# Optimization experiments

Measured on AMD Instinct MI355X. Metric: run time of the kernel, lower is better.

## Reference

```python
import jax, jax.numpy as jnp
import numpy as np


def _lstm(x_seq, W, U, b, h0, c0):
    """Keras-default LSTM. x_seq: [B,T,F]. Gate order i,f,g,o.
    Returns (all hidden states [B,T,H], final h [B,H], final c [B,H])."""
    H = U.shape[0]
    # precompute input projections for all timesteps: [T,B,4H]
    xz = jnp.einsum('btf,fg->tbg', x_seq, W) + b

    def step(carry, xz_t):
        h, c = carry
        z = xz_t + h @ U  # [B,4H]
        i = jax.nn.sigmoid(z[:, 0 * H:1 * H])
        f = jax.nn.sigmoid(z[:, 1 * H:2 * H])
        g = jnp.tanh(z[:, 2 * H:3 * H])
        o = jax.nn.sigmoid(z[:, 3 * H:4 * H])
        c = f * c + i * g
        h = o * jnp.tanh(c)
        return (h, c), h

    (hT, cT), hs = jax.lax.scan(step, (h0, c0), xz)
    return jnp.transpose(hs, (1, 0, 2)), hT, cT  # [B,T,H], [B,H], [B,H]


def setup_inputs() -> dict:
    key = jax.random.key(0)
    ks = jax.random.split(key, 7)
    B, T, F, H, C = 128, 512, 128, 512, 10
    s_in1 = 1.0 / np.sqrt(F)
    s_h = 1.0 / np.sqrt(H)
    return {
        'x': jax.random.normal(ks[0], (B, T, F), jnp.float32),
        'W1': jax.random.normal(ks[1], (F, 4 * H), jnp.float32) * s_in1,
        'U1': jax.random.normal(ks[2], (H, 4 * H), jnp.float32) * s_h,
        'b1': jnp.zeros((4 * H,), jnp.float32),
        'W2': jax.random.normal(ks[3], (H, 4 * H), jnp.float32) * s_h,
        'U2': jax.random.normal(ks[4], (H, 4 * H), jnp.float32) * s_h,
        'b2': jnp.zeros((4 * H,), jnp.float32),
        'Wd': jax.random.normal(ks[5], (H, C), jnp.float32) * s_h,
        'bd': jnp.zeros((C,), jnp.float32),
    }


def reference(x, W1, U1, b1, W2, U2, b2, Wd, bd):
    B = x.shape[0]
    H = U1.shape[0]
    h0 = jnp.zeros((B, H), x.dtype)
    c0 = jnp.zeros((B, H), x.dtype)
    # lstm1: return_sequences + return_state
    seq, h1, c1 = _lstm(x, W1, U1, b1, h0, c0)
    # Keras RNN called on [seq, h, c] uses (h, c) as lstm2's initial state
    _, h2, _ = _lstm(seq, W2, U2, b2, h1, c1)
    logits = h2 @ Wd + bd
    return jax.nn.softmax(logits, axis=-1)
```

## Files before the change

### kernel.cpp

```cpp
#include <hip/hip_runtime.h>
#include <math.h>

#define BB 128
#define TT 512
#define FF 128
#define HH 512
#define NR 2048
#define HB (HH*BB)
#define FLS 16

typedef __attribute__((ext_vector_type(8))) short short8;
typedef __attribute__((ext_vector_type(4))) float f32x4;
typedef unsigned int uint;
typedef unsigned short ushort;
typedef unsigned long long u64;

#define MFMA __builtin_amdgcn_mfma_f32_16x16x32_bf16
#define AT_LD(p)   __hip_atomic_load((p), __ATOMIC_RELAXED, __HIP_MEMORY_SCOPE_AGENT)
#define AT_ST(p,v) __hip_atomic_store((p), (v), __ATOMIC_RELAXED, __HIP_MEMORY_SCOPE_AGENT)
#define PLD(p)     (*(p))

__device__ __forceinline__ ushort f2bf(float f) {
  uint u = __float_as_uint(f);
  u += 0x7fff + ((u >> 16) & 1);
  return (ushort)(u >> 16);
}
__device__ __forceinline__ float bfh(ushort h) { return __uint_as_float(((uint)h) << 16); }
__device__ __forceinline__ u64 pk2f(float a, float b) {
  return ((u64)__float_as_uint(b) << 32) | (u64)__float_as_uint(a);
}
__device__ __forceinline__ float ftanh(float v) {
  float t = __expf(2.f * v);
  return 1.f - 2.f / (t + 1.f);
}
__device__ __forceinline__ void split8(const uint* w, short8& bh, short8& bl) {
  union { short8 v; uint d[4]; } H, Lo;
#pragma unroll
  for (int d = 0; d < 4; ++d) {
    H.d[d]  = __builtin_amdgcn_perm(w[2 * d + 1], w[2 * d], 0x07060302u);
    Lo.d[d] = __builtin_amdgcn_perm(w[2 * d + 1], w[2 * d], 0x05040100u);
  }
  bh = H.v; bl = Lo.v;
}


__global__ __launch_bounds__(256) void k_zero(float* __restrict__ p, int n) {
  int i = blockIdx.x * 256 + threadIdx.x;
  if (i < n) p[i] = 0.f;
}

__global__ __launch_bounds__(256) void k_rearr_b(const float* __restrict__ src,
                                                 float* __restrict__ dst) {
  int idx = blockIdx.x * 256 + threadIdx.x;
  int j = idx & 511, g = idx >> 9;
  dst[j * 4 + g] = src[idx];
}

__global__ __launch_bounds__(256) void k_pack_A(const float* __restrict__ src,
                                                ushort* __restrict__ dst, int ktsh) {
  int idx = blockIdx.x * 256 + threadIdx.x;
  int KTm1 = (1 << ktsh) - 1;
  int j8 = idx & 7;
  int L = (idx >> 3) & 63;
  int kt = (idx >> 9) & KTm1;
  int jb = idx >> (9 + ktsh);
  int k = kt * 32 + (L >> 4) * 8 + j8;
  int m = L & 15;
  int j = jb * 4 + (m >> 2);
  int g = m & 3;
  float v = src[(size_t)k * NR + g * HH + j];
  ushort hi = f2bf(v);
  ushort lo = f2bf(v - bfh(hi));
  size_t base = ((size_t)((jb << ktsh) + kt) * 64 + L) * 16;
  dst[base + j8] = hi;
  dst[base + 8 + j8] = lo;
}

__global__ __launch_bounds__(256, 1) void k_fused(
    const float* __restrict__ x,
    const ushort* __restrict__ W1pk, const ushort* __restrict__ U1pk,
    const float* __restrict__ bp1,
    const ushort* __restrict__ W2pk, const ushort* __restrict__ U2pk,
    const float* __restrict__ bp2,
    uint* __restrict__ seq, uint* __restrict__ ring,
    float4* __restrict__ xzr,
    int* __restrict__ hflags, int* __restrict__ pflags) {
  int tid = threadIdx.x;
  int L = tid & 63;
  int w = tid >> 6;
  int q = L >> 4, n = L & 15;
  bool isrec = (blockIdx.x < 128);
  int b = isrec ? blockIdx.x : (blockIdx.x - 128);
  int ch = b & 3, jb4 = b >> 2;
  int jbp = jb4 * 4 + w;
  int j = jbp * 4 + q;
  int col0 = ch * 32 + n;
  int pidx = b * FLS;

  short8 uh[16], ul[16];

#define RECCT(COLC, CREF, X0, X1, X2, X3, LD, WORD) {                    \
    f32x4 A0 = {0.f, 0.f, 0.f, 0.f}, A1 = A0, A2 = A0;                   \
    if (G != 0) {                                                        \
      uint wv[16][8];                                                    \
      const uint* hc = hsrc + (size_t)(q * 8) * BB + (COLC);             \
      _Pragma("unroll")                                                  \
      for (int kt = 0; kt < 16; ++kt)                                    \
        _Pragma("unroll")                                                \
        for (int u = 0; u < 8; ++u)                                      \
          wv[kt][u] = LD(hc + (size_t)(kt * 32 + u) * BB);               \
      _Pragma("unroll")                                                  \
      for (int kt = 0; kt < 16; ++kt) {                                  \
        short8 bh, bl;                                                   \
        split8(wv[kt], bh, bl);                                          \
        A0 = MFMA(uh[kt], bh, A0, 0, 0, 0);                              \
        A1 = MFMA(ul[kt], bh, A1, 0, 0, 0);                              \
        A2 = MFMA(uh[kt], bl, A2, 0, 0, 0);                              \
      }                                                                  \
    }                                                                    \
    float z0 = A0.x + A1.x + A2.x + (X0);                                \
    float z1 = A0.y + A1.y + A2.y + (X1);                                \
    float z2 = A0.z + A1.z + A2.z + (X2);                                \
    float z3 = A0.w + A1.w + A2.w + (X3);                                \
    float ig = 1.f / (1.f + __expf(-z0));                                \
    float fg = 1.f / (1.f + __expf(-z1));                                \
    float gg = ftanh(z2);                                                \
    float og = 1.f / (1.f + __expf(-z3));                                \
    (CREF) = fg * (CREF) + ig * gg;                                      \
    float hn = og * ftanh(CREF);                                         \
    ushort hh = f2bf(hn);                                                \
    (WORD) = (((uint)hh) << 16) | (uint)f2bf(hn - bfh(hh));              \
  }

  if (isrec) {
#pragma unroll
    for (int kt = 0; kt < 16; ++kt) {
      const ushort* p = U1pk + (((size_t)jbp * 16 + kt) * 64 + L) * 16;
      uh[kt] = *(const short8*)(p); ul[kt] = *(const short8*)(p + 8);
    }
    float c0 = 0.f, c1 = 0.f;
    int fidx = ((L & 31) * 4 + ch) * FLS;

#pragma unroll 1
    for (int G = 0; G < 2 * TT; ++G) {
      if (G == TT) {
#pragma unroll
        for (int kt = 0; kt < 16; ++kt) {
          const ushort* p = U2pk + (((size_t)jbp * 16 + kt) * 64 + L) * 16;
          uh[kt] = *(const short8*)(p); ul[kt] = *(const short8*)(p + 8);
        }
      }
      while (true) {
        int hf = AT_LD(hflags + fidx);
        int pf = AT_LD(pflags + pidx);
        if (__all((hf >= G) && (pf >= G + 1))) break;
      }
      asm volatile("" ::: "memory");
      const u64* xpa = (const u64*)(xzr + ((size_t)(G & 7) * HB + (size_t)j * BB + col0));
      const u64* xpb = (const u64*)(xzr + ((size_t)(G & 7) * HB + (size_t)j * BB + col0 + 16));
      u64 qa0 = AT_LD(xpa), qa1 = AT_LD(xpa + 1);
      u64 qb0 = AT_LD(xpb), qb1 = AT_LD(xpb + 1);
      float xz00 = __uint_as_float((uint)qa0), xz01 = __uint_as_float((uint)(qa0 >> 32));
      float xz02 = __uint_as_float((uint)qa1), xz03 = __uint_as_float((uint)(qa1 >> 32));
      float xz10 = __uint_as_float((uint)qb0), xz11 = __uint_as_float((uint)(qb0 >> 32));
      float xz12 = __uint_as_float((uint)qb1), xz13 = __uint_as_float((uint)(qb1 >> 32));

      uint wd0, wd1;
      if (G < TT) {
        const uint* hsrc = seq + (size_t)(G - 1) * HB;
        RECCT(col0,      c0, xz00, xz01, xz02, xz03, PLD, wd0);
        RECCT(col0 + 16, c1, xz10, xz11, xz12, xz13, PLD, wd1);
        AT_ST(&seq[(size_t)G * HB + (size_t)j * BB + col0], wd0);
        AT_ST(&seq[(size_t)G * HB + (size_t)j * BB + col0 + 16], wd1);
        if (G == TT - 1) {
          AT_ST(&ring[(size_t)3 * HB + (size_t)j * BB + col0], wd0);
          AT_ST(&ring[(size_t)3 * HB + (size_t)j * BB + col0 + 16], wd1);
        }
      } else {
        const uint* hsrc = ring + (size_t)((G - 1) & 3) * HB;
        RECCT(col0,      c0, xz00, xz01, xz02, xz03, AT_LD, wd0);
        RECCT(col0 + 16, c1, xz10, xz11, xz12, xz13, AT_LD, wd1);
        AT_ST(&ring[(size_t)(G & 3) * HB + (size_t)j * BB + col0], wd0);
        AT_ST(&ring[(size_t)(G & 3) * HB + (size_t)j * BB + col0 + 16], wd1);
      }
      __syncthreads();
      if (tid == 0) AT_ST(hflags + pidx, G + 1);
    }
  } else {
#pragma unroll
    for (int kt = 0; kt < 4; ++kt) {
      const ushort* p = W1pk + (((size_t)jbp * 4 + kt) * 64 + L) * 16;
      uh[kt] = *(const short8*)(p); ul[kt] = *(const short8*)(p + 8);
    }
    float4 bv = *(const float4*)(bp1 + j * 4);

#define PROJA(COLC) {                                                    \
    f32x4 P0 = {0.f, 0.f, 0.f, 0.f}, P1 = P0, P2 = P0;                   \
    const float* xp = x + ((size_t)(COLC) * TT + G) * FF + q * 8;        \
    _Pragma("unroll")                                                    \
    for (int kt = 0; kt < 4; ++kt) {                                     \
      float4 v0 = *(const float4*)(xp + kt * 32);                        \
      float4 v1 = *(const float4*)(xp + kt * 32 + 4);                    \
      float xf[8] = {v0.x, v0.y, v0.z, v0.w, v1.x, v1.y, v1.z, v1.w};    \
      short8 xh, xl;                                                     \
      _Pragma("unroll")                                                  \
      for (int u = 0; u < 8; ++u) {                                      \
        ushort hi = f2bf(xf[u]);                                         \
        xl[u] = (short)f2bf(xf[u] - bfh(hi));                            \
        xh[u] = (short)hi;                                               \
      }                                                                  \
      P0 = MFMA(uh[kt], xh, P0, 0, 0, 0);                                \
      P1 = MFMA(ul[kt], xh, P1, 0, 0, 0);                                \
      P2 = MFMA(uh[kt], xl, P2, 0, 0, 0);                                \
    }                                                                    \
    float o0 = P0.x + P1.x + P2.x + bv.x;                                \
    float o1 = P0.y + P1.y + P2.y + bv.y;                                \
    float o2 = P0.z + P1.z + P2.z + bv.z;                                \
    float o3 = P0.w + P1.w + P2.w + bv.w;                                \
    u64* dp = (u64*)(xzr + ((size_t)(G & 7) * HB + (size_t)j * BB + (COLC))); \
    AT_ST(dp, pk2f(o0, o1));                                             \
    AT_ST(dp + 1, pk2f(o2, o3));                                         \
  }

#define PROJB(COLC) {                                                    \
    f32x4 P0 = {0.f, 0.f, 0.f, 0.f}, P1 = P0, P2 = P0;                   \
    uint wv[16][8];                                                      \
    const uint* hc = seq + (size_t)sp * HB + (size_t)(q * 8) * BB + (COLC); \
    _Pragma("unroll")                                                    \
    for (int kt = 0; kt < 16; ++kt)                                      \
      _Pragma("unroll")                                                  \
      for (int u = 0; u < 8; ++u)                                        \
        wv[kt][u] = hc[(size_t)(kt * 32 + u) * BB];                      \
    _Pragma("unroll")                                                    \
    for (int kt = 0; kt < 16; ++kt) {                                    \
      short8 bh, bl;                                                     \
      split8(wv[kt], bh, bl);                                            \
      P0 = MFMA(uh[kt], bh, P0, 0, 0, 0);                                \
      P1 = MFMA(ul[kt], bh, P1, 0, 0, 0);                                \
      P2 = MFMA(uh[kt], bl, P2, 0, 0, 0);                                \
    }                                                                    \
    float o0 = P0.x + P1.x + P2.x + bv.x;                                \
    float o1 = P0.y + P1.y + P2.y + bv.y;                                \
    float o2 = P0.z + P1.z + P2.z + bv.z;                                \
    float o3 = P0.w + P1.w + P2.w + bv.w;                                \
    u64* dp = (u64*)(xzr + ((size_t)(G & 7) * HB + (size_t)j * BB + (COLC))); \
    AT_ST(dp, pk2f(o0, o1));                                             \
    AT_ST(dp + 1, pk2f(o2, o3));                                         \
  }

#pragma unroll 1
    for (int G = 0; G < 2 * TT; ++G) {
      if (G == TT) {
#pragma unroll
        for (int kt = 0; kt < 16; ++kt) {
          const ushort* p = W2pk + (((size_t)jbp * 16 + kt) * 64 + L) * 16;
          uh[kt] = *(const short8*)(p); ul[kt] = *(const short8*)(p + 8);
        }
        bv = *(const float4*)(bp2 + j * 4);
      }
      if (G >= 8) {
        while (AT_LD(hflags + pidx) < G - 7) __builtin_amdgcn_s_sleep(1);
      }
      asm volatile("" ::: "memory");
      if (G < TT) {
        PROJA(col0);
        PROJA(col0 + 16);
      } else {
        int sp = G - TT;
        PROJB(col0);
        PROJB(col0 + 16);
      }
      __syncthreads();
      if (tid == 0) AT_ST(pflags + pidx, G + 1);
    }
  }
}

__global__ __launch_bounds__(64) void k_dense(const uint* __restrict__ h2,
                                              const float* __restrict__ Wd,
                                              const float* __restrict__ bd,
                                              float* __restrict__ out) {
  int b = blockIdx.x * 64 + threadIdx.x;
  float acc[10];
#pragma unroll
  for (int c = 0; c < 10; ++c) acc[c] = bd[c];
  for (int k = 0; k < HH; ++k) {
    uint w = h2[k * BB + b];
    float hv = __uint_as_float(w & 0xffff0000u) + __uint_as_float(w << 16);
#pragma unroll
    for (int c = 0; c < 10; ++c) acc[c] = fmaf(hv, Wd[k * 10 + c], acc[c]);
  }
  float m = acc[0];
#pragma unroll
  for (int c = 1; c < 10; ++c) m = fmaxf(m, acc[c]);
  float s = 0.f;
#pragma unroll
  for (int c = 0; c < 10; ++c) { acc[c] = __expf(acc[c] - m); s += acc[c]; }
  float inv = 1.f / s;
#pragma unroll
  for (int c = 0; c < 10; ++c) out[b * 10 + c] = acc[c] * inv;
}

extern "C" void kernel_launch(void* const* d_in, const int* in_sizes, int n_in,
                              void* d_out, int out_size, void* d_ws, size_t ws_size,
                              hipStream_t stream) {
  const float* x  = (const float*)d_in[0];
  const float* W1 = (const float*)d_in[1];
  const float* U1 = (const float*)d_in[2];
  const float* b1 = (const float*)d_in[3];
  const float* W2 = (const float*)d_in[4];
  const float* U2 = (const float*)d_in[5];
  const float* b2 = (const float*)d_in[6];
  const float* Wd = (const float*)d_in[7];
  const float* bd = (const float*)d_in[8];
  float* out = (float*)d_out;

  uint*   seq   = (uint*)d_ws;
  uint*   ring  = seq + (size_t)TT * HB;
  float4* xzr   = (float4*)(ring + (size_t)4 * HB);
  ushort* W1pk  = (ushort*)(xzr + (size_t)8 * HB);
  ushort* U1pk  = W1pk + (size_t)524288;
  ushort* U2pk  = U1pk + (size_t)2097152;
  ushort* W2pk  = U2pk + (size_t)2097152;
  float*  bp1   = (float*)(W2pk + (size_t)2097152);
  float*  bp2   = bp1 + NR;
  int*    hflags = (int*)(bp2 + NR);
  int*    pflags = hflags + 128 * FLS;

  k_zero<<<16, 256, 0, stream>>>((float*)hflags, 2 * 128 * FLS);
  k_rearr_b<<<8, 256, 0, stream>>>(b1, bp1);
  k_rearr_b<<<8, 256, 0, stream>>>(b2, bp2);
  k_pack_A<<<1024, 256, 0, stream>>>(W1, W1pk, 2);
  k_pack_A<<<4096, 256, 0, stream>>>(U1, U1pk, 4);
  k_pack_A<<<4096, 256, 0, stream>>>(U2, U2pk, 4);
  k_pack_A<<<4096, 256, 0, stream>>>(W2, W2pk, 4);

  k_fused<<<256, 256, 0, stream>>>(x, W1pk, U1pk, bp1, W2pk, U2pk, bp2,
                                   seq, ring, xzr, hflags, pflags);
  k_dense<<<2, 64, 0, stream>>>(ring + (size_t)3 * HB, Wd, bd, out);
}
```

Baseline: 5.715 ms.

## Split recurrent matmul K dimension across wave pairs with LDS partial-sum exchange

```diff
diff --git a/kernel.cpp b/kernel.cpp
--- a/kernel.cpp
+++ b/kernel.cpp
@@ -89,43 +89,57 @@
   int L = tid & 63;
   int w = tid >> 6;
   int q = L >> 4, n = L & 15;
+  int h = w & 1, p = w >> 1;
   bool isrec = (blockIdx.x < 128);
   int b = isrec ? blockIdx.x : (blockIdx.x - 128);
   int ch = b & 3, jb4 = b >> 2;
-  int jbp = jb4 * 4 + w;
-  int j = jbp * 4 + q;
+  int rt0 = jb4 * 4 + 2 * p;
+  int jbp_own = rt0 + h;
+  int j_own = jbp_own * 4 + q;
   int col0 = ch * 32 + n;
   int pidx = b * FLS;
-
-  short8 uh[16], ul[16];
-
-#define RECCT(COLC, CREF, X0, X1, X2, X3, LD, WORD) {                    \
-    f32x4 A0 = {0.f, 0.f, 0.f, 0.f}, A1 = A0, A2 = A0;                   \
-    if (G != 0) {                                                        \
-      uint wv[16][8];                                                    \
-      const uint* hc = hsrc + (size_t)(q * 8) * BB + (COLC);             \
+  int rgive = 2 * p + 1 - h;
+  int rkeep = 2 * p + h;
+
+  __shared__ f32x4 xch[4][2][64];
+
+  short8 uh[2][8], ul[2][8];
+
+#define LOADMM(HS, LD, COLC, ZP) {                                       \
+    uint wv[8][8];                                                       \
+    const uint* hc = (HS) + (size_t)(q * 8) * BB + (COLC);               \
+    _Pragma("unroll")                                                    \
+    for (int kk = 0; kk < 8; ++kk)                                       \
       _Pragma("unroll")                                                  \
-      for (int kt = 0; kt < 16; ++kt)                                    \
-        _Pragma("unroll")                                                \
-        for (int u = 0; u < 8; ++u)                                      \
-          wv[kt][u] = LD(hc + (size_t)(kt * 32 + u) * BB);               \
+      for (int u = 0; u < 8; ++u)                                        \
+        wv[kk][u] = LD(hc + (size_t)(kk * 32 + u) * BB);                 \
+    f32x4 A0[2], A1[2], A2[2];                                           \
+    _Pragma("unroll")                                                    \
+    for (int r = 0; r < 2; ++r) {                                        \
+      A0[r] = (f32x4){0.f, 0.f, 0.f, 0.f}; A1[r] = A0[r]; A2[r] = A0[r]; \
+    }                                                                    \
+    _Pragma("unroll")                                                    \
+    for (int kk = 0; kk < 8; ++kk) {                                     \
+      short8 bh, bl;                                                     \
+      split8(wv[kk], bh, bl);                                            \
       _Pragma("unroll")                                                  \
-      for (int kt = 0; kt < 16; ++kt) {                                  \
-        short8 bh, bl;                                                   \
-        split8(wv[kt], bh, bl);                                          \
-        A0 = MFMA(uh[kt], bh, A0, 0, 0, 0);                              \
-        A1 = MFMA(ul[kt], bh, A1, 0, 0, 0);                              \
-        A2 = MFMA(uh[kt], bl, A2, 0, 0, 0);                              \
+      for (int r = 0; r < 2; ++r) {                                      \
+        A0[r] = MFMA(uh[r][kk], bh, A0[r], 0, 0, 0);                     \
+        A1[r] = MFMA(ul[r][kk], bh, A1[r], 0, 0, 0);                     \
+        A2[r] = MFMA(uh[r][kk], bl, A2[r], 0, 0, 0);                     \
       }                                                                  \
     }                                                                    \
-    float z0 = A0.x + A1.x + A2.x + (X0);                                \
-    float z1 = A0.y + A1.y + A2.y + (X1);                                \
-    float z2 = A0.z + A1.z + A2.z + (X2);                                \
-    float z3 = A0.w + A1.w + A2.w + (X3);                                \
-    float ig = 1.f / (1.f + __expf(-z0));                                \
-    float fg = 1.f / (1.f + __expf(-z1));                                \
-    float gg = ftanh(z2);                                                \
-    float og = 1.f / (1.f + __expf(-z3));                                \
+    ZP[0] = A0[0] + A1[0] + A2[0];                                       \
+    ZP[1] = A0[1] + A1[1] + A2[1];                                       \
+  }
+
+#define ACT(ZV, X0, X1, X2, X3, CREF, WORD) {                            \
+    float z0_ = (ZV).x + (X0), z1_ = (ZV).y + (X1);                      \
+    float z2_ = (ZV).z + (X2), z3_ = (ZV).w + (X3);                      \
+    float ig = 1.f / (1.f + __expf(-z0_));                               \
+    float fg = 1.f / (1.f + __expf(-z1_));                               \
+    float gg = ftanh(z2_);                                               \
+    float og = 1.f / (1.f + __expf(-z3_));                               \
     (CREF) = fg * (CREF) + ig * gg;                                      \
     float hn = og * ftanh(CREF);                                         \
     ushort hh = f2bf(hn);                                                \
@@ -134,21 +148,25 @@
 
   if (isrec) {
 #pragma unroll
-    for (int kt = 0; kt < 16; ++kt) {
-      const ushort* p = U1pk + (((size_t)jbp * 16 + kt) * 64 + L) * 16;
-      uh[kt] = *(const short8*)(p); ul[kt] = *(const short8*)(p + 8);
-    }
+    for (int r = 0; r < 2; ++r)
+#pragma unroll
+      for (int kk = 0; kk < 8; ++kk) {
+        const ushort* pp = U1pk + (((size_t)(rt0 + r) * 16 + (8 * h + kk)) * 64 + L) * 16;
+        uh[r][kk] = *(const short8*)(pp); ul[r][kk] = *(const short8*)(pp + 8);
+      }
     float c0 = 0.f, c1 = 0.f;
-    int fidx = ((L & 31) * 4 + ch) * FLS;
+    int fidx = ((16 * h + (L & 15)) * 4 + ch) * FLS;
 
 #pragma unroll 1
     for (int G = 0; G < 2 * TT; ++G) {
       if (G == TT) {
 #pragma unroll
-        for (int kt = 0; kt < 16; ++kt) {
-          const ushort* p = U2pk + (((size_t)jbp * 16 + kt) * 64 + L) * 16;
-          uh[kt] = *(const short8*)(p); ul[kt] = *(const short8*)(p + 8);
-        }
+        for (int r = 0; r < 2; ++r)
+#pragma unroll
+          for (int kk = 0; kk < 8; ++kk) {
+            const ushort* pp = U2pk + (((size_t)(rt0 + r) * 16 + (8 * h + kk)) * 64 + L) * 16;
+            uh[r][kk] = *(const short8*)(pp); ul[r][kk] = *(const short8*)(pp + 8);
+          }
       }
       while (true) {
         int hf = AT_LD(hflags + fidx);
@@ -156,119 +174,134 @@
         if (__all((hf >= G) && (pf >= G + 1))) break;
       }
       asm volatile("" ::: "memory");
-      const u64* xpa = (const u64*)(xzr + ((size_t)(G & 7) * HB + (size_t)j * BB + col0));
-      const u64* xpb = (const u64*)(xzr + ((size_t)(G & 7) * HB + (size_t)j * BB + col0 + 16));
+      const u64* xpa = (const u64*)(xzr + ((size_t)(G & 7) * HB + (size_t)j_own * BB + col0));
+      const u64* xpb = (const u64*)(xzr + ((size_t)(G & 7) * HB + (size_t)j_own * BB + col0 + 16));
       u64 qa0 = AT_LD(xpa), qa1 = AT_LD(xpa + 1);
       u64 qb0 = AT_LD(xpb), qb1 = AT_LD(xpb + 1);
-      float xz00 = __uint_as_float((uint)qa0), xz01 = __uint_as_float((uint)(qa0 >> 32));
-      float xz02 = __uint_as_float((uint)qa1), xz03 = __uint_as_float((uint)(qa1 >> 32));
-      float xz10 = __uint_as_float((uint)qb0), xz11 = __uint_as_float((uint)(qb0 >> 32));
-      float xz12 = __uint_as_float((uint)qb1), xz13 = __uint_as_float((uint)(qb1 >> 32));
-
-      uint wd0, wd1;
-      if (G < TT) {
-        const uint* hsrc = seq + (size_t)(G - 1) * HB;
-        RECCT(col0,      c0, xz00, xz01, xz02, xz03, PLD, wd0);
-        RECCT(col0 + 16, c1, xz10, xz11, xz12, xz13, PLD, wd1);
-        AT_ST(&seq[(size_t)G * HB + (size_t)j * BB + col0], wd0);
-        AT_ST(&seq[(size_t)G * HB + (size_t)j * BB + col0 + 16], wd1);
-        if (G == TT - 1) {
-          AT_ST(&ring[(size_t)3 * HB + (size_t)j * BB + col0], wd0);
-          AT_ST(&ring[(size_t)3 * HB + (size_t)j * BB + col0 + 16], wd1);
+
+      f32x4 zp0[2], zp1[2];
+      if (G != 0) {
+        if (G < TT) {
+          const uint* hs = seq + (size_t)(G - 1) * HB + (size_t)(256 * h) * BB;
+          LOADMM(hs, PLD, col0, zp0);
+          LOADMM(hs, PLD, col0 + 16, zp1);
+        } else {
+          const uint* hs = ring + (size_t)((G - 1) & 3) * HB + (size_t)(256 * h) * BB;
+          LOADMM(hs, AT_LD, col0, zp0);
+          LOADMM(hs, AT_LD, col0 + 16, zp1);
         }
       } else {
-        const uint* hsrc = ring + (size_t)((G - 1) & 3) * HB;
-        RECCT(col0,      c0, xz00, xz01, xz02, xz03, AT_LD, wd0);
-        RECCT(col0 + 16, c1, xz10, xz11, xz12, xz13, AT_LD, wd1);
-        AT_ST(&ring[(size_t)(G & 3) * HB + (size_t)j * BB + col0], wd0);
-        AT_ST(&ring[(size_t)(G & 3) * HB + (size_t)j * BB + col0 + 16], wd1);
+        zp0[0] = (f32x4){0.f, 0.f, 0.f, 0.f}; zp0[1] = zp0[0];
+        zp1[0] = zp0[0]; zp1[1] = zp0[0];
+      }
+      xch[rgive][0][L] = h ? zp0[0] : zp0[1];
+      xch[rgive][1][L] = h ? zp1[0] : zp1[1];
+      __syncthreads();
+      f32x4 z0 = (h ? zp0[1] : zp0[0]) + xch[rkeep][0][L];
+      f32x4 z1 = (h ? zp1[1] : zp1[0]) + xch[rkeep][1][L];
+
+      uint wd0, wd1;
+      ACT(z0, __uint_as_float((uint)qa0), __uint_as_float((uint)(qa0 >> 32)),
+          __uint_as_float((uint)qa1), __uint_as_float((uint)(qa1 >> 32)), c0, wd0);
+      ACT(z1, __uint_as_float((uint)qb0), __uint_as_float((uint)(qb0 >> 32)),
+          __uint_as_float((uint)qb1), __uint_as_float((uint)(qb1 >> 32)), c1, wd1);
+
+      if (G < TT) {
+        AT_ST(&seq[(size_t)G * HB + (size_t)j_own * BB + col0], wd0);
+        AT_ST(&seq[(size_t)G * HB + (size_t)j_own * BB + col0 + 16], wd1);
+        if (G == TT - 1) {
+          AT_ST(&ring[(size_t)3 * HB + (size_t)j_own * BB + col0], wd0);
+          AT_ST(&ring[(size_t)3 * HB + (size_t)j_own * BB + col0 + 16], wd1);
+        }
+      } else {
+        AT_ST(&ring[(size_t)(G & 3) * HB + (size_t)j_own * BB + col0], wd0);
+        AT_ST(&ring[(size_t)(G & 3) * HB + (size_t)j_own * BB + col0 + 16], wd1);
       }
       __syncthreads();
       if (tid == 0) AT_ST(hflags + pidx, G + 1);
     }
   } else {
 #pragma unroll
-    for (int kt = 0; kt < 4; ++kt) {
-      const ushort* p = W1pk + (((size_t)jbp * 4 + kt) * 64 + L) * 16;
-      uh[kt] = *(const short8*)(p); ul[kt] = *(const short8*)(p + 8);
-    }
-    float4 bv = *(const float4*)(bp1 + j * 4);
-
-#define PROJA(COLC) {                                                    \
-    f32x4 P0 = {0.f, 0.f, 0.f, 0.f}, P1 = P0, P2 = P0;                   \
-    const float* xp = x + ((size_t)(COLC) * TT + G) * FF + q * 8;        \
-    _Pragma("unroll")                                                    \
-    for (int kt = 0; kt < 4; ++kt) {                                     \
-      float4 v0 = *(const float4*)(xp + kt * 32);                        \
-      float4 v1 = *(const float4*)(xp + kt * 32 + 4);                    \
-      float xf[8] = {v0.x, v0.y, v0.z, v0.w, v1.x, v1.y, v1.z, v1.w};    \
-      short8 xh, xl;                                                     \
-      _Pragma("unroll")                                                  \
-      for (int u = 0; u < 8; ++u) {                                      \
-        ushort hi = f2bf(xf[u]);                                         \
-        xl[u] = (short)f2bf(xf[u] - bfh(hi));                            \
-        xh[u] = (short)hi;                                               \
-      }                                                                  \
-      P0 = MFMA(uh[kt], xh, P0, 0, 0, 0);                                \
-      P1 = MFMA(ul[kt], xh, P1, 0, 0, 0);                                \
-      P2 = MFMA(uh[kt], xl, P2, 0, 0, 0);                                \
-    }                                                                    \
-    float o0 = P0.x + P1.x + P2.x + bv.x;                                \
-    float o1 = P0.y + P1.y + P2.y + bv.y;                                \
-    float o2 = P0.z + P1.z + P2.z + bv.z;                                \
-    float o3 = P0.w + P1.w + P2.w + bv.w;                                \
-    u64* dp = (u64*)(xzr + ((size_t)(G & 7) * HB + (size_t)j * BB + (COLC))); \
-    AT_ST(dp, pk2f(o0, o1));                                             \
-    AT_ST(dp + 1, pk2f(o2, o3));                                         \
-  }
-
-#define PROJB(COLC) {                                                    \
-    f32x4 P0 = {0.f, 0.f, 0.f, 0.f}, P1 = P0, P2 = P0;                   \
-    uint wv[16][8];                                                      \
-    const uint* hc = seq + (size_t)sp * HB + (size_t)(q * 8) * BB + (COLC); \
-    _Pragma("unroll")                                                    \
-    for (int kt = 0; kt < 16; ++kt)                                      \
-      _Pragma("unroll")                                                  \
-      for (int u = 0; u < 8; ++u)                                        \
-        wv[kt][u] = hc[(size_t)(kt * 32 + u) * BB];                      \
-    _Pragma("unroll")                                                    \
-    for (int kt = 0; kt < 16; ++kt) {                                    \
-      short8 bh, bl;                                                     \
-      split8(wv[kt], bh, bl);                                            \
-      P0 = MFMA(uh[kt], bh, P0, 0, 0, 0);                                \
-      P1 = MFMA(ul[kt], bh, P1, 0, 0, 0);                                \
-      P2 = MFMA(uh[kt], bl, P2, 0, 0, 0);                                \
-    }                                                                    \
-    float o0 = P0.x + P1.x + P2.x + bv.x;                                \
-    float o1 = P0.y + P1.y + P2.y + bv.y;                                \
-    float o2 = P0.z + P1.z + P2.z + bv.z;                                \
-    float o3 = P0.w + P1.w + P2.w + bv.w;                                \
-    u64* dp = (u64*)(xzr + ((size_t)(G & 7) * HB + (size_t)j * BB + (COLC))); \
-    AT_ST(dp, pk2f(o0, o1));                                             \
-    AT_ST(dp + 1, pk2f(o2, o3));                                         \
-  }
+    for (int r = 0; r < 2; ++r)
+#pragma unroll
+      for (int kk = 0; kk < 2; ++kk) {
+        const ushort* pp = W1pk + (((size_t)(rt0 + r) * 4 + (2 * h + kk)) * 64 + L) * 16;
+        uh[r][kk] = *(const short8*)(pp); ul[r][kk] = *(const short8*)(pp + 8);
+      }
+    float4 bv = *(const float4*)(bp1 + j_own * 4);
 
 #pragma unroll 1
     for (int G = 0; G < 2 * TT; ++G) {
       if (G == TT) {
 #pragma unroll
-        for (int kt = 0; kt < 16; ++kt) {
-          const ushort* p = W2pk + (((size_t)jbp * 16 + kt) * 64 + L) * 16;
-          uh[kt] = *(const short8*)(p); ul[kt] = *(const short8*)(p + 8);
-        }
-        bv = *(const float4*)(bp2 + j * 4);
+        for (int r = 0; r < 2; ++r)
+#pragma unroll
+          for (int kk = 0; kk < 8; ++kk) {
+            const ushort* pp = W2pk + (((size_t)(rt0 + r) * 16 + (8 * h + kk)) * 64 + L) * 16;
+            uh[r][kk] = *(const short8*)(pp); ul[r][kk] = *(const short8*)(pp + 8);
+          }
+        bv = *(const float4*)(bp2 + j_own * 4);
       }
       if (G >= 8) {
         while (AT_LD(hflags + pidx) < G - 7) __builtin_amdgcn_s_sleep(1);
       }
       asm volatile("" ::: "memory");
+
+      f32x4 zp0[2], zp1[2];
       if (G < TT) {
-        PROJA(col0);
-        PROJA(col0 + 16);
+#pragma unroll
+        for (int r = 0; r < 2; ++r) {
+          zp0[r] = (f32x4){0.f, 0.f, 0.f, 0.f}; zp1[r] = zp0[r];
+        }
+#define PROJA_CT(COLC, ZP) {                                             \
+        f32x4 P0[2], P1[2], P2[2];                                       \
+        _Pragma("unroll")                                                \
+        for (int r = 0; r < 2; ++r) {                                    \
+          P0[r] = (f32x4){0.f, 0.f, 0.f, 0.f}; P1[r] = P0[r]; P2[r] = P0[r]; \
+        }                                                                \
+        const float* xp = x + ((size_t)(COLC) * TT + G) * FF + q * 8 + 64 * h; \
+        _Pragma("unroll")                                                \
+        for (int kk = 0; kk < 2; ++kk) {                                 \
+          float4 v0 = *(const float4*)(xp + kk * 32);                    \
+          float4 v1 = *(const float4*)(xp + kk * 32 + 4);                \
+          float xf[8] = {v0.x, v0.y, v0.z, v0.w, v1.x, v1.y, v1.z, v1.w}; \
+          short8 xh, xl;                                                 \
+          _Pragma("unroll")                                              \
+          for (int u = 0; u < 8; ++u) {                                  \
+            ushort hi = f2bf(xf[u]);                                     \
+            xl[u] = (short)f2bf(xf[u] - bfh(hi));                        \
+            xh[u] = (short)hi;                                           \
+          }                                                              \
+          _Pragma("unroll")                                              \
+          for (int r = 0; r < 2; ++r) {                                  \
+            P0[r] = MFMA(uh[r][kk], xh, P0[r], 0, 0, 0);                 \
+            P1[r] = MFMA(ul[r][kk], xh, P1[r], 0, 0, 0);                 \
+            P2[r] = MFMA(uh[r][kk], xl, P2[r], 0, 0, 0);                 \
+          }                                                              \
+        }                                                                \
+        ZP[0] = P0[0] + P1[0] + P2[0];                                   \
+        ZP[1] = P0[1] + P1[1] + P2[1];                                   \
+      }
+        PROJA_CT(col0, zp0);
+        PROJA_CT(col0 + 16, zp1);
       } else {
         int sp = G - TT;
-        PROJB(col0);
-        PROJB(col0 + 16);
+        const uint* hs = seq + (size_t)sp * HB + (size_t)(256 * h) * BB;
+        LOADMM(hs, PLD, col0, zp0);
+        LOADMM(hs, PLD, col0 + 16, zp1);
+      }
+      xch[rgive][0][L] = h ? zp0[0] : zp0[1];
+      xch[rgive][1][L] = h ? zp1[0] : zp1[1];
+      __syncthreads();
+      f32x4 z0 = (h ? zp0[1] : zp0[0]) + xch[rkeep][0][L];
+      f32x4 z1 = (h ? zp1[1] : zp1[0]) + xch[rkeep][1][L];
+      {
+        u64* dp = (u64*)(xzr + ((size_t)(G & 7) * HB + (size_t)j_own * BB + col0));
+        AT_ST(dp, pk2f(z0.x + bv.x, z0.y + bv.y));
+        AT_ST(dp + 1, pk2f(z0.z + bv.z, z0.w + bv.w));
+        u64* dq = (u64*)(xzr + ((size_t)(G & 7) * HB + (size_t)j_own * BB + col0 + 16));
+        AT_ST(dq, pk2f(z1.x + bv.x, z1.y + bv.y));
+        AT_ST(dq + 1, pk2f(z1.z + bv.z, z1.w + bv.w));
       }
       __syncthreads();
       if (tid == 0) AT_ST(pflags + pidx, G + 1);
```

Measured after the change: 5.206 ms. -8.9%, faster.
